# Kernel optimization log

Hardware: AMD Instinct MI355X
Metric: run time of the kernel (lower is better)

## Reference

```python
import jax, jax.numpy as jnp
import numpy as np

D_MODEL = 1024
D_STATE = 128
HEADDIM = 64
EXPAND = 2
CHUNK = 64
D_CONV = 4
D_INNER = EXPAND * D_MODEL          # 2048
NHEADS = D_INNER // HEADDIM         # 32
D_IN_PROJ = 2 * D_INNER + 2 * D_STATE + NHEADS  # 4384
CONV_CH = D_INNER + 2 * D_STATE     # 2304
EPS = 1e-5


def segsum(x):
    # x: (..., T) -> (..., T, T); out[i, j] = sum_{k=j+1..i} x[k] for i>=j else -inf
    T = x.shape[-1]
    m1 = jnp.tril(jnp.ones((T, T), bool), -1)
    xr = jnp.where(m1, x[..., :, None], 0.0)   # zero above/at diagonal before cumsum
    s = jnp.cumsum(xr, axis=-2)
    m0 = jnp.tril(jnp.ones((T, T), bool), 0)
    return jnp.where(m0, s, -jnp.inf)


def ssd(x, A, B, C, chunk):
    # x: (b, L, h, p); A: (b, L, h); B, C: (b, L, n)  (the h=1 dim of the torch code is squeezed)
    b, L, h, p = x.shape
    c = L // chunk
    x = x.reshape(b, c, chunk, h, p)
    A = A.reshape(b, c, chunk, h).transpose(0, 3, 1, 2)  # (b, h, c, l)
    B = B.reshape(b, c, chunk, -1)                       # (b, c, l, n)
    C = C.reshape(b, c, chunk, -1)
    A_cum = jnp.cumsum(A, axis=-1)                       # (b, h, c, l)
    Lm = jnp.exp(segsum(A))                              # (b, h, c, l, l)
    # intra-chunk (diagonal block) output
    Y_diag = jnp.einsum('bcln,bcsn,bhcls,bcshp->bclhp', C, B, Lm, x)
    # per-chunk states
    decay_states = jnp.exp(A_cum[:, :, :, -1:] - A_cum)  # (b, h, c, l)
    states = jnp.einsum('bcln,bhcl,bclhp->bchpn', B, decay_states, x)
    init = jnp.zeros_like(states[:, :1])
    states = jnp.concatenate([init, states], axis=1)     # (b, c+1, h, p, n)
    # inter-chunk recurrence
    Ac_last = jnp.pad(A_cum[:, :, :, -1], ((0, 0), (0, 0), (1, 0)))  # (b, h, c+1)
    decay_chunk = jnp.exp(segsum(Ac_last))               # (b, h, c+1, c+1)
    new_states = jnp.einsum('bhzc,bchpn->bzhpn', decay_chunk, states)
    states = new_states[:, :-1]                          # (b, c, h, p, n)
    sdo = jnp.exp(A_cum)
    Y_off = jnp.einsum('bcln,bchpn,bhcl->bclhp', C, states, sdo)
    return (Y_diag + Y_off).reshape(b, L, h, p)


def setup_inputs() -> dict:
    key = jax.random.key(0)
    ks = jax.random.split(key, 8)
    return {
        'u': jax.random.normal(ks[0], (2, 4096, D_MODEL), jnp.float32),
        'W_in': jax.random.normal(ks[1], (D_MODEL, D_IN_PROJ), jnp.float32) * 0.02,
        'conv_w': jax.random.normal(ks[2], (CONV_CH, D_CONV), jnp.float32) * 0.3,
        'conv_b': jax.random.normal(ks[3], (CONV_CH,), jnp.float32) * 0.1,
        'dt_bias': jax.random.normal(ks[4], (NHEADS,), jnp.float32),
        'A_log': jax.random.normal(ks[5], (NHEADS,), jnp.float32) * 0.5,
        'D': jax.random.normal(ks[6], (NHEADS,), jnp.float32),
        'norm_w': jnp.ones((D_INNER,), jnp.float32),
        'W_out': jax.random.normal(ks[7], (D_INNER, D_MODEL), jnp.float32) * 0.02,
    }


def reference(u, W_in, conv_w, conv_b, dt_bias, A_log, D, norm_w, W_out):
    b, L, _ = u.shape
    zxbcdt = u @ W_in                                    # (b, L, 4384)
    z = zxbcdt[..., :D_INNER]
    xBC = zxbcdt[..., D_INNER:D_INNER + CONV_CH]
    dt = jax.nn.softplus(zxbcdt[..., -NHEADS:] + dt_bias)  # (b, L, h)
    # depthwise causal conv (Conv1d pad=d_conv-1, truncated to L == left-pad only)
    xc = jnp.pad(xBC.transpose(0, 2, 1), ((0, 0), (0, 0), (D_CONV - 1, 0)))
    xc = jax.lax.conv_general_dilated(
        xc, conv_w[:, None, :], (1,), 'VALID',
        feature_group_count=CONV_CH,
        dimension_numbers=('NCH', 'OIH', 'NCH')) + conv_b[None, :, None]
    xBC = jax.nn.silu(xc.transpose(0, 2, 1))             # (b, L, 2304)
    x = xBC[..., :D_INNER].reshape(b, L, NHEADS, HEADDIM)
    B = xBC[..., D_INNER:D_INNER + D_STATE]
    C = xBC[..., D_INNER + D_STATE:]
    A = -jnp.exp(A_log)                                  # (h,)
    y = ssd(x * dt[..., None], A * dt, B, C, CHUNK)
    y = y + x * D[:, None]
    y = y.reshape(b, L, D_INNER)
    # RMSNorm with gate z
    y = y * jax.nn.silu(z)
    y = y * jax.lax.rsqrt(jnp.mean(y * y, axis=-1, keepdims=True) + EPS) * norm_w
    return y @ W_out
```

## Files before the change

### kernel.cpp

```cpp
#include <hip/hip_runtime.h>
#include <hip/hip_bf16.h>
#include <math.h>

#define D_MODEL   1024
#define D_STATE   128
#define HEADDIM   64
#define CHUNK     64
#define D_INNER   2048
#define NHEADS    32
#define D_IN_PROJ 4384
#define CONV_CH   2304
#define RCOLS     2336
#define WINT_ROWS 4480
#define BATCH     2
#define SEQ       4096
#define NCHUNK    64
#define ROWS      (BATCH*SEQ)
#define EPS_RMS   1e-5f

typedef __hip_bfloat16 bf16;
typedef __bf16 bf16x8_t __attribute__((ext_vector_type(8)));
typedef float  f32x4_t  __attribute__((ext_vector_type(4)));

__device__ __forceinline__ float siluf_(float x){ return x/(1.f+expf(-x)); }
__device__ __forceinline__ float ldf(const float* p){ return *p; }
__device__ __forceinline__ float ldf(const bf16* p){ return __bfloat162float(*p); }
__device__ __forceinline__ void  stf(float* p, float v){ *p = v; }
__device__ __forceinline__ void  stf(bf16* p, float v){ *p = __float2bfloat16(v); }

__device__ __forceinline__ __bf16 tobf(float v){
    __hip_bfloat16 t = __float2bfloat16(v);
    return *reinterpret_cast<__bf16*>(&t);
}
__device__ __forceinline__ unsigned short bfbits(float v){
    __hip_bfloat16 t = __float2bfloat16(v);
    return *reinterpret_cast<unsigned short*>(&t);
}
__device__ __forceinline__ float bfbits2f(unsigned short u){
    union { unsigned u; float f; } cv; cv.u = ((unsigned)u) << 16; return cv.f;
}

__device__ __forceinline__ void async16(const void* g, void* l) {
    __builtin_amdgcn_global_load_lds(
        (const __attribute__((address_space(1))) unsigned int*)g,
        (__attribute__((address_space(3))) unsigned int*)l, 16, 0, 0);
}

struct Core {
    f32x4_t acc[4][4];

    __device__ __forceinline__ void stA2(const bf16* __restrict__ A, int lda,
                                         int row0, int kk, __bf16* Asb,
                                         int tid, int lcb, int wb, int c0) {
#pragma unroll
        for (int c = c0; c < c0 + 2; ++c) {
            const char* src = (const char*)(A + (size_t)(row0 + c * 64 + (tid >> 3)) * lda + kk) + lcb;
            async16(src, Asb + c * 4096 + wb);
        }
    }
    __device__ __forceinline__ void stB2(const bf16* __restrict__ Bt, int ldb,
                                         int col0, int kk, __bf16* Bsb,
                                         int tid, int lcb, int wb) {
#pragma unroll
        for (int c = 0; c < 2; ++c) {
            const char* src = (const char*)(Bt + (size_t)(col0 + c * 64 + (tid >> 3)) * ldb + kk) + lcb;
            async16(src, Bsb + c * 4096 + wb);
        }
    }

    __device__ __forceinline__ void run(const bf16* __restrict__ A,
                                        const bf16* __restrict__ Bt,
                                        int lda, int ldb,
                                        int row0, int col0, int k0, int nt,
                                        __bf16* As, __bf16* Bs, int tid) {
        const int wave = tid >> 6, lane = tid & 63;
        const int quad = lane >> 4, l16 = lane & 15;
        const int wm = wave >> 1, wn = wave & 1;
        const int wb  = wave << 9;
        const int lcb = (((tid & 7) ^ ((tid >> 3) & 7)) << 4);
        const int xb = (l16 & 7) << 4;

#pragma unroll
        for (int i = 0; i < 4; ++i)
#pragma unroll
            for (int j = 0; j < 4; ++j) acc[i][j] = (f32x4_t){0.f, 0.f, 0.f, 0.f};

        int aoff[4][2], boff[4][2];
#pragma unroll
        for (int mi = 0; mi < 4; ++mi)
#pragma unroll
            for (int ks = 0; ks < 2; ++ks) {
                const int cb = ((ks << 6) | (quad << 4)) ^ xb;
                aoff[mi][ks] = (wm * 64 + mi * 16 + l16) * 128 + cb;
                boff[mi][ks] = (wn * 64 + mi * 16 + l16) * 128 + cb;
            }

        stA2(A, lda, row0, k0, As, tid, lcb, wb, 0);
        stA2(A, lda, row0, k0, As, tid, lcb, wb, 2);
        stB2(Bt, ldb, col0, k0, Bs, tid, lcb, wb);
        stA2(A, lda, row0, k0 + 64, As + 16384, tid, lcb, wb, 0);
        stA2(A, lda, row0, k0 + 64, As + 16384, tid, lcb, wb, 2);
        stB2(Bt, ldb, col0, k0 + 64, Bs + 8192, tid, lcb, wb);

        const char* AsC = (const char*)As;
        const char* BsC = (const char*)Bs;
        int cur = 0;
        for (int t = 0; t < nt; ++t) {
            if (t < nt - 1) asm volatile("s_waitcnt vmcnt(6)" ::: "memory");
            else            asm volatile("s_waitcnt vmcnt(0)" ::: "memory");
            __builtin_amdgcn_s_barrier();
            asm volatile("" ::: "memory");

            const int sb = (cur + 2 >= 3) ? cur - 1 : cur + 2;
            const bool st = (t + 2 < nt);
            const int kk = k0 + (t + 2) * 64;
            const char* Ab = AsC + cur * 32768;
            const char* Bb = BsC + cur * 16384;
            __bf16* Asb = As + sb * 16384;
            __bf16* Bsb = Bs + sb * 8192;

            bf16x8_t af0[2][2], af1[2][2], bf0[2][2], bf1[2][2];

#pragma unroll
            for (int i = 0; i < 2; ++i)
#pragma unroll
                for (int ks = 0; ks < 2; ++ks) {
                    af0[i][ks] = *(const bf16x8_t*)(Ab + aoff[i][ks]);
                    bf0[i][ks] = *(const bf16x8_t*)(Bb + boff[i][ks]);
                }
            if (st) stA2(A, lda, row0, kk, Asb, tid, lcb, wb, 0);
            asm volatile("" ::: "memory");
            __builtin_amdgcn_s_barrier();
            asm volatile("" ::: "memory");
            __builtin_amdgcn_s_setprio(1);
#pragma unroll
            for (int ks = 0; ks < 2; ++ks)
#pragma unroll
                for (int mi = 0; mi < 2; ++mi)
#pragma unroll
                    for (int ni = 0; ni < 2; ++ni)
                        acc[mi][ni] = __builtin_amdgcn_mfma_f32_16x16x32_bf16(
                            af0[mi][ks], bf0[ni][ks], acc[mi][ni], 0, 0, 0);
            __builtin_amdgcn_s_setprio(0);

#pragma unroll
            for (int i = 0; i < 2; ++i)
#pragma unroll
                for (int ks = 0; ks < 2; ++ks)
                    bf1[i][ks] = *(const bf16x8_t*)(Bb + boff[2 + i][ks]);
            if (st) stA2(A, lda, row0, kk, Asb, tid, lcb, wb, 2);
            asm volatile("" ::: "memory");
            __builtin_amdgcn_s_barrier();
            asm volatile("" ::: "memory");
            __builtin_amdgcn_s_setprio(1);
#pragma unroll
            for (int ks = 0; ks < 2; ++ks)
#pragma unroll
                for (int mi = 0; mi < 2; ++mi)
#pragma unroll
                    for (int ni = 0; ni < 2; ++ni)
                        acc[mi][2 + ni] = __builtin_amdgcn_mfma_f32_16x16x32_bf16(
                            af0[mi][ks], bf1[ni][ks], acc[mi][2 + ni], 0, 0, 0);
            __builtin_amdgcn_s_setprio(0);

#pragma unroll
            for (int i = 0; i < 2; ++i)
#pragma unroll
                for (int ks = 0; ks < 2; ++ks)
                    af1[i][ks] = *(const bf16x8_t*)(Ab + aoff[2 + i][ks]);
            if (st) stB2(Bt, ldb, col0, kk, Bsb, tid, lcb, wb);
            asm volatile("" ::: "memory");
            __builtin_amdgcn_s_barrier();
            asm volatile("" ::: "memory");
            __builtin_amdgcn_s_setprio(1);
#pragma unroll
            for (int ks = 0; ks < 2; ++ks)
#pragma unroll
                for (int mi = 0; mi < 2; ++mi) {
#pragma unroll
                    for (int ni = 0; ni < 2; ++ni)
                        acc[2 + mi][2 + ni] = __builtin_amdgcn_mfma_f32_16x16x32_bf16(
                            af1[mi][ks], bf1[ni][ks], acc[2 + mi][2 + ni], 0, 0, 0);
#pragma unroll
                    for (int ni = 0; ni < 2; ++ni)
                        acc[2 + mi][ni] = __builtin_amdgcn_mfma_f32_16x16x32_bf16(
                            af1[mi][ks], bf0[ni][ks], acc[2 + mi][ni], 0, 0, 0);
                }
            __builtin_amdgcn_s_setprio(0);

            cur = (cur + 1 == 3) ? 0 : cur + 1;
        }
    }
};

__global__ __launch_bounds__(512) void gemm_zr_fused(const bf16* __restrict__ A,
                                                     const bf16* __restrict__ Bt,
                                                     bf16* __restrict__ Z,
                                                     bf16* __restrict__ R) {
    __shared__ __align__(16) __bf16 As[3 * 16384];
    __shared__ __align__(16) __bf16 Bs[3 * 8192];
    const int tid = threadIdx.x;
    const int row0 = blockIdx.x * 256;
    const int ct   = blockIdx.y;
    Core g;
    g.run(A, Bt, D_MODEL, D_MODEL, row0, ct * 128, 0, 16, As, Bs, tid);

    const int wave = tid >> 6, lane = tid & 63;
    const int quad = lane >> 4, l16 = lane & 15;
    const int wm = wave >> 1, wn = wave & 1;
    bf16* Cp; int ldc_, cl0, ncols;
    if (ct < 16) { Cp = Z; ldc_ = D_INNER; cl0 = ct * 128;           ncols = D_INNER; }
    else         { Cp = R; ldc_ = RCOLS;   cl0 = ct * 128 - D_INNER; ncols = RCOLS; }
#pragma unroll
    for (int ni = 0; ni < 4; ++ni) {
        int gc = cl0 + wn * 64 + ni * 16 + l16;
        if (gc >= ncols) continue;
#pragma unroll
        for (int mi = 0; mi < 4; ++mi)
#pragma unroll
            for (int r = 0; r < 4; ++r) {
                int gr = row0 + wm * 64 + mi * 16 + quad * 4 + r;
                stf(&Cp[(size_t)gr * ldc_ + gc], g.acc[mi][ni][r]);
            }
    }
}

__global__ __launch_bounds__(512) void gemm_out_kernel(const bf16* __restrict__ A,
                                                       const bf16* __restrict__ Bt,
                                                       float* __restrict__ out) {
    __shared__ __align__(16) __bf16 As[3 * 16384];
    __shared__ __align__(16) __bf16 Bs[3 * 8192];
    const int tid = threadIdx.x;
    const int row0 = blockIdx.x * 256;
    const int col0 = blockIdx.y * 128;
    Core g;
    g.run(A, Bt, D_INNER, D_INNER, row0, col0, 0, 32, As, Bs, tid);

    const int wave = tid >> 6, lane = tid & 63;
    const int quad = lane >> 4, l16 = lane & 15;
    const int wm = wave >> 1, wn = wave & 1;
#pragma unroll
    for (int ni = 0; ni < 4; ++ni) {
        int gc = col0 + wn * 64 + ni * 16 + l16;
#pragma unroll
        for (int mi = 0; mi < 4; ++mi)
#pragma unroll
            for (int r = 0; r < 4; ++r) {
                int gr = row0 + wm * 64 + mi * 16 + quad * 4 + r;
                out[(size_t)gr * D_MODEL + gc] = g.acc[mi][ni][r];
            }
    }
}

__global__ void cvt_bf16_kernel(const float* __restrict__ src,
                                bf16* __restrict__ dst, int n4) {
    int i = blockIdx.x * 256 + threadIdx.x;
    if (i >= n4) return;
    float4 v = ((const float4*)src)[i];
    dst[i * 4 + 0] = __float2bfloat16(v.x);
    dst[i * 4 + 1] = __float2bfloat16(v.y);
    dst[i * 4 + 2] = __float2bfloat16(v.z);
    dst[i * 4 + 3] = __float2bfloat16(v.w);
}

__global__ __launch_bounds__(256) void transpose_cvt_kernel(const float* __restrict__ W,
                                                            bf16* __restrict__ Wt,
                                                            int R, int C, int Cpad) {
    __shared__ float tile[32][33];
    int c0 = blockIdx.x * 32, r0 = blockIdx.y * 32;
    int tx = threadIdx.x & 31, ty = threadIdx.x >> 5;
    for (int i = ty; i < 32; i += 8) {
        int r = r0 + i, c = c0 + tx;
        tile[i][tx] = (c < C) ? W[(size_t)r * C + c] : 0.f;
    }
    __syncthreads();
    for (int i = ty; i < 32; i += 8) {
        int c = c0 + i, r = r0 + tx;
        stf(&Wt[(size_t)c * R + r], tile[tx][i]);
    }
}

__global__ void prep_convw_kernel(const float* __restrict__ conv_w,
                                  bf16* __restrict__ Wc) {
    int i = blockIdx.x * 256 + threadIdx.x;
    if (i >= CONV_CH * 4) return;
    int ch = i >> 2, k = i & 3;
    Wc[k * CONV_CH + ch] = __float2bfloat16(conv_w[ch * 4 + k]);
}

__global__ __launch_bounds__(256) void conv_silu_kernel(const bf16* __restrict__ R,
                                                        const bf16* __restrict__ Wc,
                                                        const float* __restrict__ conv_b,
                                                        bf16* __restrict__ xBC) {
    int idx = blockIdx.x * 256 + threadIdx.x;
    int rq = idx / 288;
    int g = idx - rq * 288;
    int ch0 = g * 8;
    int row0 = rq * 4;
    int l0 = row0 & (SEQ - 1);

    uint4 rv[7];
#pragma unroll
    for (int j = 0; j < 7; ++j) {
        int ls = l0 - 3 + j;
        rv[j] = (ls >= 0) ? *(const uint4*)&R[(size_t)(row0 - 3 + j) * RCOLS + ch0]
                          : make_uint4(0u, 0u, 0u, 0u);
    }
    uint4 wv[4];
#pragma unroll
    for (int k = 0; k < 4; ++k)
        wv[k] = *(const uint4*)&Wc[k * CONV_CH + ch0];
    float4 b0 = ((const float4*)conv_b)[ch0 / 4];
    float4 b1 = ((const float4*)conv_b)[ch0 / 4 + 1];
    const float bias[8] = {b0.x, b0.y, b0.z, b0.w, b1.x, b1.y, b1.z, b1.w};
    float wf[4][8];
#pragma unroll
    for (int k = 0; k < 4; ++k) {
        const unsigned* wp = (const unsigned*)&wv[k];
#pragma unroll
        for (int j2 = 0; j2 < 4; ++j2) {
            wf[k][2 * j2]     = bfbits2f((unsigned short)(wp[j2] & 0xffff));
            wf[k][2 * j2 + 1] = bfbits2f((unsigned short)(wp[j2] >> 16));
        }
    }
#pragma unroll
    for (int j = 0; j < 4; ++j) {
        float acc[8];
#pragma unroll
        for (int cc = 0; cc < 8; ++cc) acc[cc] = bias[cc];
#pragma unroll
        for (int k = 0; k < 4; ++k) {
            const unsigned* vp = (const unsigned*)&rv[j + k];
#pragma unroll
            for (int j2 = 0; j2 < 4; ++j2) {
                unsigned v = vp[j2];
                acc[2 * j2]     += wf[k][2 * j2]     * bfbits2f((unsigned short)(v & 0xffff));
                acc[2 * j2 + 1] += wf[k][2 * j2 + 1] * bfbits2f((unsigned short)(v >> 16));
            }
        }
        unsigned o[4];
#pragma unroll
        for (int j2 = 0; j2 < 4; ++j2)
            o[j2] = (unsigned)bfbits(siluf_(acc[2 * j2])) |
                    ((unsigned)bfbits(siluf_(acc[2 * j2 + 1])) << 16);
        *(uint4*)&xBC[(size_t)(row0 + j) * CONV_CH + ch0] = make_uint4(o[0], o[1], o[2], o[3]);
    }
}

__global__ void dt_kernel(const bf16* __restrict__ R,
                          const float* __restrict__ dt_bias,
                          float* __restrict__ dtb) {
    int i = blockIdx.x * 256 + threadIdx.x;
    int row = i >> 2, h0 = (i & 3) * 8;
    uint4 v = *(const uint4*)&R[(size_t)row * RCOLS + CONV_CH + h0];
    float4 bia0 = ((const float4*)dt_bias)[h0 / 4];
    float4 bia1 = ((const float4*)dt_bias)[h0 / 4 + 1];
    const unsigned vv[4] = {v.x, v.y, v.z, v.w};
    const float bb[8] = {bia0.x, bia0.y, bia0.z, bia0.w, bia1.x, bia1.y, bia1.z, bia1.w};
    float o[8];
#pragma unroll
    for (int j = 0; j < 4; ++j) {
        float a = bfbits2f((unsigned short)(vv[j] & 0xffff)) + bb[2*j];
        float c = bfbits2f((unsigned short)(vv[j] >> 16)) + bb[2*j+1];
        o[2*j]   = (a > 20.f) ? a : log1pf(expf(a));
        o[2*j+1] = (c > 20.f) ? c : log1pf(expf(c));
    }
    float* dp = &dtb[(size_t)row * NHEADS + h0];
    *(float4*)dp       = make_float4(o[0], o[1], o[2], o[3]);
    *(float4*)(dp + 4) = make_float4(o[4], o[5], o[6], o[7]);
}

__global__ void acum_kernel(const float* __restrict__ dtb,
                            const float* __restrict__ A_log,
                            float* __restrict__ Acum) {
    int bch = blockIdx.x;
    int h = bch & 31;
    int bc = bch >> 5;
    int c = bc & 63, b = bc >> 6;
    int row0 = b * SEQ + c * CHUNK;
    __shared__ float sh[64];
    int l = threadIdx.x;
    float Ah = -expf(A_log[h]);
    sh[l] = Ah * dtb[(size_t)(row0 + l) * NHEADS + h];
    __syncthreads();
    float s = 0.f;
    for (int j = 0; j <= l; ++j) s += sh[j];
    Acum[(size_t)bch * 64 + l] = s;
}

__global__ __launch_bounds__(64) void gchunk_mfma_kernel(const bf16* __restrict__ xBC,
                                                         float* __restrict__ Gbuf) {
    int bc = blockIdx.x;
    int c = bc & 63, b = bc >> 6;
    int row0 = b * SEQ + c * CHUNK;
    int lane = threadIdx.x;
    int quad = lane >> 4, l16 = lane & 15;

    f32x4_t acc[4][4];
#pragma unroll
    for (int i = 0; i < 4; ++i)
#pragma unroll
        for (int j = 0; j < 4; ++j) acc[i][j] = (f32x4_t){0.f, 0.f, 0.f, 0.f};

#pragma unroll
    for (int ks = 0; ks < 4; ++ks) {
        bf16x8_t a[4], bb[4];
#pragma unroll
        for (int mi = 0; mi < 4; ++mi)
            a[mi] = *(const bf16x8_t*)&xBC[(size_t)(row0 + mi * 16 + l16) * CONV_CH +
                                           D_INNER + D_STATE + ks * 32 + quad * 8];
#pragma unroll
        for (int ni = 0; ni < 4; ++ni)
            bb[ni] = *(const bf16x8_t*)&xBC[(size_t)(row0 + ni * 16 + l16) * CONV_CH +
                                            D_INNER + ks * 32 + quad * 8];
#pragma unroll
        for (int mi = 0; mi < 4; ++mi)
#pragma unroll
            for (int ni = 0; ni < 4; ++ni)
                acc[mi][ni] = __builtin_amdgcn_mfma_f32_16x16x32_bf16(
                    a[mi], bb[ni], acc[mi][ni], 0, 0, 0);
    }
#pragma unroll
    for (int ni = 0; ni < 4; ++ni) {
        int s = ni * 16 + l16;
#pragma unroll
        for (int mi = 0; mi < 4; ++mi)
#pragma unroll
            for (int r = 0; r < 4; ++r) {
                int l = mi * 16 + quad * 4 + r;
                Gbuf[(size_t)bc * 4096 + l * 64 + s] = acc[mi][ni][r];
            }
    }
}

__global__ __launch_bounds__(256) void states_mfma_kernel(const bf16* __restrict__ xBC,
                                                          const float* __restrict__ dtb,
                                                          const float* __restrict__ Acum,
                                                          bf16* __restrict__ states) {
    __shared__ __align__(16) __bf16 BsT[128 * 72];
    __shared__ __align__(16) __bf16 xdT[4][64 * 72];
    __shared__ float dtdec[4][64];
    int bcq = blockIdx.x;
    int hq = bcq & 7, bc = bcq >> 3;
    int c = bc & 63, b = bc >> 6;
    int tid = threadIdx.x, wave = tid >> 6, lane = tid & 63;
    int h = hq * 4 + wave;
    int bch = bc * 32 + h;
    int row0 = b * SEQ + c * CHUNK;
    int quad = lane >> 4, l16 = lane & 15;

    {
        float alast = Acum[(size_t)bch * 64 + 63];
        float a = Acum[(size_t)bch * 64 + lane];
        dtdec[wave][lane] = dtb[(size_t)(row0 + lane) * NHEADS + h] * expf(alast - a);
    }
    __syncthreads();
    for (int it = 0; it < 16; ++it) {
        int i2 = tid + 256 * it;
        int l = i2 >> 6;
        int n0 = (i2 & 63) * 2;
        unsigned v = *(const unsigned*)&xBC[(size_t)(row0 + l) * CONV_CH + D_INNER + n0];
        *(unsigned short*)&BsT[(n0    ) * 72 + l] = (unsigned short)(v & 0xffff);
        *(unsigned short*)&BsT[(n0 + 1) * 72 + l] = (unsigned short)(v >> 16);
    }
    for (int it = 0; it < 32; ++it) {
        int l = 2 * it + (lane >> 5);
        int p0 = (lane & 31) * 2;
        unsigned v = *(const unsigned*)&xBC[(size_t)(row0 + l) * CONV_CH + h * 64 + p0];
        float f = dtdec[wave][l];
        xdT[wave][(p0    ) * 72 + l] = tobf(bfbits2f((unsigned short)(v & 0xffff)) * f);
        xdT[wave][(p0 + 1) * 72 + l] = tobf(bfbits2f((unsigned short)(v >> 16)) * f);
    }
    __syncthreads();

    f32x4_t acc[4][8];
#pragma unroll
    for (int i = 0; i < 4; ++i)
#pragma unroll
        for (int j = 0; j < 8; ++j) acc[i][j] = (f32x4_t){0.f, 0.f, 0.f, 0.f};
#pragma unroll
    for (int ks = 0; ks < 2; ++ks) {
        bf16x8_t a[4], bb[8];
#pragma unroll
        for (int mi = 0; mi < 4; ++mi)
            a[mi] = *(const bf16x8_t*)(&xdT[wave][(mi * 16 + l16) * 72 + ks * 32 + quad * 8]);
#pragma unroll
        for (int ni = 0; ni < 8; ++ni)
            bb[ni] = *(const bf16x8_t*)(&BsT[(ni * 16 + l16) * 72 + ks * 32 + quad * 8]);
#pragma unroll
        for (int mi = 0; mi < 4; ++mi)
#pragma unroll
            for (int ni = 0; ni < 8; ++ni)
                acc[mi][ni] = __builtin_amdgcn_mfma_f32_16x16x32_bf16(
                    a[mi], bb[ni], acc[mi][ni], 0, 0, 0);
    }
#pragma unroll
    for (int ni = 0; ni < 8; ++ni) {
        int n = ni * 16 + l16;
#pragma unroll
        for (int mi = 0; mi < 4; ++mi)
#pragma unroll
            for (int r = 0; r < 4; ++r) {
                int p = mi * 16 + quad * 4 + r;
                stf(&states[(size_t)bch * 8192 + p * 128 + n], acc[mi][ni][r]);
            }
    }
}

__global__ void scan_kernel(const float* __restrict__ Acum,
                            bf16* __restrict__ states) {
    int i = blockIdx.x * 256 + threadIdx.x;
    int pn0 = (i & 2047) * 4;
    int bh = i >> 11;
    int h = bh & 31, b = bh >> 5;
    float carry[4] = {0.f, 0.f, 0.f, 0.f};
    for (int c = 0; c < NCHUNK; ++c) {
        int bch = (b * NCHUNK + c) * NHEADS + h;
        bf16* sp = &states[(size_t)bch * 8192 + pn0];
        uint2 v = *(const uint2*)sp;
        float s0 = bfbits2f((unsigned short)(v.x & 0xffff));
        float s1 = bfbits2f((unsigned short)(v.x >> 16));
        float s2 = bfbits2f((unsigned short)(v.y & 0xffff));
        float s3 = bfbits2f((unsigned short)(v.y >> 16));
        uint2 o;
        o.x = (unsigned)bfbits(carry[0]) | ((unsigned)bfbits(carry[1]) << 16);
        o.y = (unsigned)bfbits(carry[2]) | ((unsigned)bfbits(carry[3]) << 16);
        *(uint2*)sp = o;
        float dec = expf(Acum[(size_t)bch * 64 + 63]);
        carry[0] = carry[0] * dec + s0;
        carry[1] = carry[1] * dec + s1;
        carry[2] = carry[2] * dec + s2;
        carry[3] = carry[3] * dec + s3;
    }
}

__global__ __launch_bounds__(64) void y_mfma_kernel(const bf16* __restrict__ xBC,
                                                    const float* __restrict__ dtb,
                                                    const float* __restrict__ Acum,
                                                    const float* __restrict__ Gbuf,
                                                    const bf16* __restrict__ states,
                                                    const float* __restrict__ Dv,
                                                    bf16* __restrict__ y) {
    __shared__ __align__(16) __bf16 Mm[64 * 72];
    __shared__ __align__(16) __bf16 xsT[64 * 72];
    __shared__ float acs[64], dtss[64], sdos[64];
    int bch = blockIdx.x;
    int h = bch & 31, bc = bch >> 5;
    int c = bc & 63, b = bc >> 6;
    int row0 = b * SEQ + c * CHUNK;
    int lane = threadIdx.x;
    int quad = lane >> 4, l16 = lane & 15;

    {
        float a = Acum[(size_t)bch * 64 + lane];
        acs[lane] = a;
        sdos[lane] = expf(a);
        dtss[lane] = dtb[(size_t)(row0 + lane) * NHEADS + h];
    }
    __syncthreads();
    for (int l = 0; l < 64; ++l) {
        int s = lane;
        float d = acs[l] - acs[s];
        float g = (s <= l) ? Gbuf[(size_t)bc * 4096 + l * 64 + s] * dtss[s] : 0.f;
        float coef = g * expf((s <= l) ? d : 0.f);
        Mm[l * 72 + s] = tobf(coef);
    }
    for (int it = 0; it < 32; ++it) {
        int l = 2 * it + (lane >> 5);
        int p0 = (lane & 31) * 2;
        unsigned v = *(const unsigned*)&xBC[(size_t)(row0 + l) * CONV_CH + h * 64 + p0];
        *(unsigned short*)&xsT[(p0    ) * 72 + l] = (unsigned short)(v & 0xffff);
        *(unsigned short*)&xsT[(p0 + 1) * 72 + l] = (unsigned short)(v >> 16);
    }
    __syncthreads();

    f32x4_t acc[4][4];
#pragma unroll
    for (int i = 0; i < 4; ++i)
#pragma unroll
        for (int j = 0; j < 4; ++j) acc[i][j] = (f32x4_t){0.f, 0.f, 0.f, 0.f};

#pragma unroll
    for (int ks = 0; ks < 2; ++ks) {
        bf16x8_t a[4], bb[4];
#pragma unroll
        for (int mi = 0; mi < 4; ++mi)
            a[mi] = *(const bf16x8_t*)(&Mm[(mi * 16 + l16) * 72 + ks * 32 + quad * 8]);
#pragma unroll
        for (int ni = 0; ni < 4; ++ni)
            bb[ni] = *(const bf16x8_t*)(&xsT[(ni * 16 + l16) * 72 + ks * 32 + quad * 8]);
#pragma unroll
        for (int mi = 0; mi < 4; ++mi)
#pragma unroll
            for (int ni = 0; ni < 4; ++ni)
                acc[mi][ni] = __builtin_amdgcn_mfma_f32_16x16x32_bf16(
                    a[mi], bb[ni], acc[mi][ni], 0, 0, 0);
    }
    float sdo_mi[4];
#pragma unroll
    for (int mi = 0; mi < 4; ++mi) sdo_mi[mi] = sdos[mi * 16 + l16];
#pragma unroll
    for (int ks = 0; ks < 4; ++ks) {
        bf16x8_t a[4], bb[4];
#pragma unroll
        for (int mi = 0; mi < 4; ++mi) {
            const unsigned* cp = (const unsigned*)&xBC[(size_t)(row0 + mi * 16 + l16) * CONV_CH
                                                       + D_INNER + D_STATE + ks * 32 + quad * 8];
            float sc = sdo_mi[mi];
#pragma unroll
            for (int jj = 0; jj < 4; ++jj) {
                unsigned v = cp[jj];
                a[mi][2 * jj    ] = tobf(bfbits2f((unsigned short)(v & 0xffff)) * sc);
                a[mi][2 * jj + 1] = tobf(bfbits2f((unsigned short)(v >> 16)) * sc);
            }
        }
#pragma unroll
        for (int ni = 0; ni < 4; ++ni)
            bb[ni] = *(const bf16x8_t*)&states[(size_t)bch * 8192 + (ni * 16 + l16) * 128
                                               + ks * 32 + quad * 8];
#pragma unroll
        for (int mi = 0; mi < 4; ++mi)
#pragma unroll
            for (int ni = 0; ni < 4; ++ni)
                acc[mi][ni] = __builtin_amdgcn_mfma_f32_16x16x32_bf16(
                    a[mi], bb[ni], acc[mi][ni], 0, 0, 0);
    }
    float Dh = Dv[h];
#pragma unroll
    for (int ni = 0; ni < 4; ++ni) {
        int p = ni * 16 + l16;
#pragma unroll
        for (int mi = 0; mi < 4; ++mi)
#pragma unroll
            for (int r = 0; r < 4; ++r) {
                int l = mi * 16 + quad * 4 + r;
                float xv = bfbits2f(*(const unsigned short*)&xsT[p * 72 + l]);
                stf(&y[(size_t)(row0 + l) * D_INNER + h * 64 + p],
                    acc[mi][ni][r] + Dh * xv);
            }
    }
}

__global__ __launch_bounds__(256) void gate_norm_kernel(const bf16* __restrict__ Z,
                                                        const float* __restrict__ nw,
                                                        bf16* __restrict__ y) {
    int row = blockIdx.x;
    int tid = threadIdx.x;
    int col0 = tid * 8;
    uint4 zv = *(const uint4*)&Z[(size_t)row * D_INNER + col0];
    uint4 yv = *(const uint4*)&y[(size_t)row * D_INNER + col0];
    const unsigned zz[4] = {zv.x, zv.y, zv.z, zv.w};
    const unsigned yy[4] = {yv.x, yv.y, yv.z, yv.w};
    float vals[8];
    float local = 0.f;
#pragma unroll
    for (int j = 0; j < 4; ++j) {
        float z0 = bfbits2f((unsigned short)(zz[j] & 0xffff));
        float z1 = bfbits2f((unsigned short)(zz[j] >> 16));
        float y0 = bfbits2f((unsigned short)(yy[j] & 0xffff));
        float y1 = bfbits2f((unsigned short)(yy[j] >> 16));
        float v0 = y0 * siluf_(z0);
        float v1 = y1 * siluf_(z1);
        vals[2*j] = v0; vals[2*j+1] = v1;
        local += v0 * v0 + v1 * v1;
    }
#pragma unroll
    for (int off = 32; off; off >>= 1) local += __shfl_down(local, off, 64);
    __shared__ float wsum[4];
    if ((tid & 63) == 0) wsum[tid >> 6] = local;
    __syncthreads();
    float total = wsum[0] + wsum[1] + wsum[2] + wsum[3];
    float scale = rsqrtf(total / (float)D_INNER + EPS_RMS);
    float4 w0 = ((const float4*)nw)[col0 / 4];
    float4 w1 = ((const float4*)nw)[col0 / 4 + 1];
    const float ww[8] = {w0.x, w0.y, w0.z, w0.w, w1.x, w1.y, w1.z, w1.w};
    unsigned o[4];
#pragma unroll
    for (int j = 0; j < 4; ++j)
        o[j] = (unsigned)bfbits(vals[2*j] * scale * ww[2*j]) |
               ((unsigned)bfbits(vals[2*j+1] * scale * ww[2*j+1]) << 16);
    *(uint4*)&y[(size_t)row * D_INNER + col0] = make_uint4(o[0], o[1], o[2], o[3]);
}

extern "C" void kernel_launch(void* const* d_in, const int* in_sizes, int n_in,
                              void* d_out, int out_size, void* d_ws, size_t ws_size,
                              hipStream_t stream) {
    const float* u       = (const float*)d_in[0];
    const float* W_in    = (const float*)d_in[1];
    const float* conv_w  = (const float*)d_in[2];
    const float* conv_b  = (const float*)d_in[3];
    const float* dt_bias = (const float*)d_in[4];
    const float* A_log   = (const float*)d_in[5];
    const float* Dv      = (const float*)d_in[6];
    const float* norm_w  = (const float*)d_in[7];
    const float* W_out   = (const float*)d_in[8];
    float* out = (float*)d_out;

    const size_t sz_xBC    = (size_t)ROWS * CONV_CH * 2;
    const size_t sz_Z      = (size_t)ROWS * D_INNER * 2;
    const size_t sz_y      = (size_t)ROWS * D_INNER * 2;
    const size_t sz_states = (size_t)BATCH * NCHUNK * NHEADS * 8192 * 2;
    const size_t sz_dtb    = (size_t)ROWS * NHEADS * 4;
    const size_t sz_Acum   = (size_t)BATCH * NCHUNK * NHEADS * 64 * 4;
    const size_t sz_Gbuf   = (size_t)BATCH * NCHUNK * 4096 * 4;
    const size_t sz_WinT   = (size_t)WINT_ROWS * D_MODEL * 2;
    const size_t sz_WoutT  = (size_t)D_MODEL * D_INNER * 2;
    const size_t sz_Wc     = (size_t)CONV_CH * 4 * 2;
    const size_t need = sz_xBC + sz_Z + sz_y + sz_states + sz_dtb + sz_Acum +
                        sz_Gbuf + sz_WinT + sz_WoutT + sz_Wc;
    if (ws_size < need) {
        hipMemsetAsync(d_out, 0, (size_t)out_size * sizeof(float), stream);
        return;
    }
    char* ws = (char*)d_ws;
    size_t off = 0;
    bf16*  xBC    = (bf16*) (ws + off); off += sz_xBC;
    bf16*  Z      = (bf16*) (ws + off); off += sz_Z;
    bf16*  y      = (bf16*) (ws + off); off += sz_y;
    bf16*  states = (bf16*) (ws + off); off += sz_states;
    float* dtb    = (float*)(ws + off); off += sz_dtb;
    float* Acum   = (float*)(ws + off); off += sz_Acum;
    float* Gbuf   = (float*)(ws + off); off += sz_Gbuf;
    bf16*  W_inT  = (bf16*) (ws + off); off += sz_WinT;
    bf16*  W_outT = (bf16*) (ws + off); off += sz_WoutT;
    bf16*  Wc     = (bf16*) (ws + off); off += sz_Wc;
    bf16*  R        = states;
    bf16*  u_bf16   = (bf16*)((char*)states + (size_t)ROWS * RCOLS * 2);

    cvt_bf16_kernel<<<(ROWS * D_MODEL / 4 + 255) / 256, 256, 0, stream>>>(
        u, u_bf16, ROWS * D_MODEL / 4);
    transpose_cvt_kernel<<<dim3(WINT_ROWS / 32, D_MODEL / 32), 256, 0, stream>>>(
        W_in, W_inT, D_MODEL, D_IN_PROJ, WINT_ROWS);
    transpose_cvt_kernel<<<dim3(D_MODEL / 32, D_INNER / 32), 256, 0, stream>>>(
        W_out, W_outT, D_INNER, D_MODEL, D_MODEL);
    prep_convw_kernel<<<(CONV_CH * 4 + 255) / 256, 256, 0, stream>>>(conv_w, Wc);
    gemm_zr_fused<<<dim3(ROWS / 256, 35), 512, 0, stream>>>(u_bf16, W_inT, Z, R);
    conv_silu_kernel<<<ROWS / 4 * 288 / 256, 256, 0, stream>>>(R, Wc, conv_b, xBC);
    dt_kernel<<<ROWS * 4 / 256, 256, 0, stream>>>(R, dt_bias, dtb);
    acum_kernel<<<BATCH * NCHUNK * NHEADS, 64, 0, stream>>>(dtb, A_log, Acum);
    gchunk_mfma_kernel<<<BATCH * NCHUNK, 64, 0, stream>>>(xBC, Gbuf);
    states_mfma_kernel<<<BATCH * NCHUNK * 8, 256, 0, stream>>>(xBC, dtb, Acum, states);
    scan_kernel<<<BATCH * NHEADS * 2048 / 256, 256, 0, stream>>>(Acum, states);
    y_mfma_kernel<<<BATCH * NCHUNK * NHEADS, 64, 0, stream>>>(
        xBC, dtb, Acum, Gbuf, states, Dv, y);
    gate_norm_kernel<<<ROWS, 256, 0, stream>>>(Z, norm_w, y);
    gemm_out_kernel<<<dim3(ROWS / 256, D_MODEL / 128), 512, 0, stream>>>(
        y, W_outT, out);
}
```

Measured before the change: 437.4 us.

## Enlarge GEMM tiles to 256x256 with double buffering and split-K output GEMM

Replaces the 256x128 triple-buffered GEMM core with a 256x256 tile using 8 waves arranged 2x4, each computing a 128x64 sub-tile, with two-stage LDS double buffering. The input-projection GEMM gets padded weight rows so it can use 256-wide column tiles. The output GEMM now splits K in two, writes fp32 partial sums into the reused states buffer, and adds a separate reduction kernel. The aim is higher arithmetic intensity per loaded tile and enough blocks to fill the GPU. The cost is more accumulator registers, which may limit occupancy, extra fp32 partial-sum traffic, one more kernel launch, and wasted compute on the padded columns.

```diff
diff --git a/kernel.cpp b/kernel.cpp
--- a/kernel.cpp
+++ b/kernel.cpp
@@ -11,7 +11,7 @@
 #define D_IN_PROJ 4384
 #define CONV_CH   2304
 #define RCOLS     2336
-#define WINT_ROWS 4480
+#define WINT_ROWS 4608
 #define BATCH     2
 #define SEQ       4096
 #define NCHUNK    64
@@ -46,26 +46,14 @@
         (__attribute__((address_space(3))) unsigned int*)l, 16, 0, 0);
 }
 
-struct Core {
-    f32x4_t acc[4][4];
-
-    __device__ __forceinline__ void stA2(const bf16* __restrict__ A, int lda,
-                                         int row0, int kk, __bf16* Asb,
-                                         int tid, int lcb, int wb, int c0) {
-#pragma unroll
-        for (int c = c0; c < c0 + 2; ++c) {
-            const char* src = (const char*)(A + (size_t)(row0 + c * 64 + (tid >> 3)) * lda + kk) + lcb;
-            async16(src, Asb + c * 4096 + wb);
-        }
-    }
-    __device__ __forceinline__ void stB2(const bf16* __restrict__ Bt, int ldb,
-                                         int col0, int kk, __bf16* Bsb,
-                                         int tid, int lcb, int wb) {
-#pragma unroll
-        for (int c = 0; c < 2; ++c) {
-            const char* src = (const char*)(Bt + (size_t)(col0 + c * 64 + (tid >> 3)) * ldb + kk) + lcb;
-            async16(src, Bsb + c * 4096 + wb);
-        }
+struct Core256 {
+    f32x4_t acc[8][4];
+
+    __device__ __forceinline__ void stg(const bf16* __restrict__ g, int ld,
+                                        int rbase, int kk, __bf16* buf, int c,
+                                        int tid, int lcb) {
+        const char* src = (const char*)(g + (size_t)(rbase + c * 64 + (tid >> 3)) * ld + kk) + lcb;
+        async16(src, buf + c * 4096 + ((tid >> 6) << 9));
     }
 
     __device__ __forceinline__ void run(const bf16* __restrict__ A,
@@ -75,120 +63,148 @@
                                         __bf16* As, __bf16* Bs, int tid) {
         const int wave = tid >> 6, lane = tid & 63;
         const int quad = lane >> 4, l16 = lane & 15;
-        const int wm = wave >> 1, wn = wave & 1;
-        const int wb  = wave << 9;
+        const int wm = wave >> 2, wn = wave & 3;
         const int lcb = (((tid & 7) ^ ((tid >> 3) & 7)) << 4);
         const int xb = (l16 & 7) << 4;
 
 #pragma unroll
-        for (int i = 0; i < 4; ++i)
+        for (int i = 0; i < 8; ++i)
 #pragma unroll
             for (int j = 0; j < 4; ++j) acc[i][j] = (f32x4_t){0.f, 0.f, 0.f, 0.f};
 
-        int aoff[4][2], boff[4][2];
-#pragma unroll
-        for (int mi = 0; mi < 4; ++mi)
-#pragma unroll
-            for (int ks = 0; ks < 2; ++ks) {
-                const int cb = ((ks << 6) | (quad << 4)) ^ xb;
-                aoff[mi][ks] = (wm * 64 + mi * 16 + l16) * 128 + cb;
-                boff[mi][ks] = (wn * 64 + mi * 16 + l16) * 128 + cb;
-            }
-
-        stA2(A, lda, row0, k0, As, tid, lcb, wb, 0);
-        stA2(A, lda, row0, k0, As, tid, lcb, wb, 2);
-        stB2(Bt, ldb, col0, k0, Bs, tid, lcb, wb);
-        stA2(A, lda, row0, k0 + 64, As + 16384, tid, lcb, wb, 0);
-        stA2(A, lda, row0, k0 + 64, As + 16384, tid, lcb, wb, 2);
-        stB2(Bt, ldb, col0, k0 + 64, Bs + 8192, tid, lcb, wb);
-
-        const char* AsC = (const char*)As;
-        const char* BsC = (const char*)Bs;
-        int cur = 0;
+        int aoff[8][2], boff[4][2];
+#pragma unroll
+        for (int ks = 0; ks < 2; ++ks) {
+            const int cb = ((ks << 6) | (quad << 4)) ^ xb;
+#pragma unroll
+            for (int mi = 0; mi < 8; ++mi)
+                aoff[mi][ks] = (wm * 128 + mi * 16 + l16) * 128 + cb;
+#pragma unroll
+            for (int ni = 0; ni < 4; ++ni)
+                boff[ni][ks] = (wn * 64 + ni * 16 + l16) * 128 + cb;
+        }
+
+        stg(A,  lda, row0, k0, As, 0, tid, lcb);
+        stg(A,  lda, row0, k0, As, 2, tid, lcb);
+        stg(Bt, ldb, col0, k0, Bs, 0, tid, lcb);
+        stg(Bt, ldb, col0, k0, Bs, 1, tid, lcb);
+        stg(Bt, ldb, col0, k0, Bs, 2, tid, lcb);
+        stg(Bt, ldb, col0, k0, Bs, 3, tid, lcb);
+        stg(A,  lda, row0, k0, As, 1, tid, lcb);
+        stg(A,  lda, row0, k0, As, 3, tid, lcb);
+        asm volatile("s_waitcnt vmcnt(2)" ::: "memory");
+        __builtin_amdgcn_s_barrier();
+        asm volatile("" ::: "memory");
+
         for (int t = 0; t < nt; ++t) {
-            if (t < nt - 1) asm volatile("s_waitcnt vmcnt(6)" ::: "memory");
-            else            asm volatile("s_waitcnt vmcnt(0)" ::: "memory");
+            const bool st = (t + 1 < nt);
+            const int kk = k0 + (t + 1) * 64;
+            const int cur = t & 1;
+            const char* Ab = (const char*)(As + cur * 16384);
+            const char* Bb = (const char*)(Bs + cur * 16384);
+            __bf16* Asb = As + (cur ^ 1) * 16384;
+            __bf16* Bsb = Bs + (cur ^ 1) * 16384;
+            bf16x8_t af[4][2], b0r[2][2], b1r[2][2];
+
+#pragma unroll
+            for (int mi = 0; mi < 4; ++mi)
+#pragma unroll
+                for (int ks = 0; ks < 2; ++ks)
+                    af[mi][ks] = *(const bf16x8_t*)(Ab + aoff[mi][ks]);
+#pragma unroll
+            for (int ni = 0; ni < 2; ++ni)
+#pragma unroll
+                for (int ks = 0; ks < 2; ++ks)
+                    b0r[ni][ks] = *(const bf16x8_t*)(Bb + boff[ni][ks]);
+            if (st) {
+                stg(A,  lda, row0, kk, Asb, 0, tid, lcb);
+                stg(A,  lda, row0, kk, Asb, 2, tid, lcb);
+                stg(Bt, ldb, col0, kk, Bsb, 0, tid, lcb);
+            }
+            asm volatile("" ::: "memory");
+            __builtin_amdgcn_s_barrier();
+            asm volatile("s_waitcnt lgkmcnt(0)" ::: "memory");
+            __builtin_amdgcn_s_setprio(1);
+#pragma unroll
+            for (int ks = 0; ks < 2; ++ks)
+#pragma unroll
+                for (int mi = 0; mi < 4; ++mi)
+#pragma unroll
+                    for (int ni = 0; ni < 2; ++ni)
+                        acc[mi][ni] = __builtin_amdgcn_mfma_f32_16x16x32_bf16(
+                            af[mi][ks], b0r[ni][ks], acc[mi][ni], 0, 0, 0);
+            __builtin_amdgcn_s_setprio(0);
             __builtin_amdgcn_s_barrier();
             asm volatile("" ::: "memory");
 
-            const int sb = (cur + 2 >= 3) ? cur - 1 : cur + 2;
-            const bool st = (t + 2 < nt);
-            const int kk = k0 + (t + 2) * 64;
-            const char* Ab = AsC + cur * 32768;
-            const char* Bb = BsC + cur * 16384;
-            __bf16* Asb = As + sb * 16384;
-            __bf16* Bsb = Bs + sb * 8192;
-
-            bf16x8_t af0[2][2], af1[2][2], bf0[2][2], bf1[2][2];
-
-#pragma unroll
-            for (int i = 0; i < 2; ++i)
-#pragma unroll
-                for (int ks = 0; ks < 2; ++ks) {
-                    af0[i][ks] = *(const bf16x8_t*)(Ab + aoff[i][ks]);
-                    bf0[i][ks] = *(const bf16x8_t*)(Bb + boff[i][ks]);
-                }
-            if (st) stA2(A, lda, row0, kk, Asb, tid, lcb, wb, 0);
+#pragma unroll
+            for (int ni = 0; ni < 2; ++ni)
+#pragma unroll
+                for (int ks = 0; ks < 2; ++ks)
+                    b1r[ni][ks] = *(const bf16x8_t*)(Bb + boff[2 + ni][ks]);
+            if (st) {
+                stg(Bt, ldb, col0, kk, Bsb, 1, tid, lcb);
+                stg(Bt, ldb, col0, kk, Bsb, 2, tid, lcb);
+                stg(Bt, ldb, col0, kk, Bsb, 3, tid, lcb);
+                asm volatile("s_waitcnt vmcnt(6)" ::: "memory");
+            } else {
+                asm volatile("s_waitcnt vmcnt(0)" ::: "memory");
+            }
+            __builtin_amdgcn_s_barrier();
+            asm volatile("s_waitcnt lgkmcnt(0)" ::: "memory");
+            __builtin_amdgcn_s_setprio(1);
+#pragma unroll
+            for (int ks = 0; ks < 2; ++ks)
+#pragma unroll
+                for (int mi = 0; mi < 4; ++mi)
+#pragma unroll
+                    for (int ni = 0; ni < 2; ++ni)
+                        acc[mi][2 + ni] = __builtin_amdgcn_mfma_f32_16x16x32_bf16(
+                            af[mi][ks], b1r[ni][ks], acc[mi][2 + ni], 0, 0, 0);
+            __builtin_amdgcn_s_setprio(0);
+            __builtin_amdgcn_s_barrier();
             asm volatile("" ::: "memory");
+
+#pragma unroll
+            for (int mi = 0; mi < 4; ++mi)
+#pragma unroll
+                for (int ks = 0; ks < 2; ++ks)
+                    af[mi][ks] = *(const bf16x8_t*)(Ab + aoff[4 + mi][ks]);
+            if (st) stg(A, lda, row0, kk, Asb, 1, tid, lcb);
+            asm volatile("" ::: "memory");
+            __builtin_amdgcn_s_barrier();
+            asm volatile("s_waitcnt lgkmcnt(0)" ::: "memory");
+            __builtin_amdgcn_s_setprio(1);
+#pragma unroll
+            for (int ks = 0; ks < 2; ++ks)
+#pragma unroll
+                for (int mi = 0; mi < 4; ++mi)
+#pragma unroll
+                    for (int ni = 0; ni < 2; ++ni)
+                        acc[4 + mi][2 + ni] = __builtin_amdgcn_mfma_f32_16x16x32_bf16(
+                            af[mi][ks], b1r[ni][ks], acc[4 + mi][2 + ni], 0, 0, 0);
+            __builtin_amdgcn_s_setprio(0);
+            __builtin_amdgcn_s_barrier();
+            asm volatile("" ::: "memory");
+
+            if (st) {
+                stg(A, lda, row0, kk, Asb, 3, tid, lcb);
+                asm volatile("s_waitcnt vmcnt(2)" ::: "memory");
+            }
             __builtin_amdgcn_s_barrier();
             asm volatile("" ::: "memory");
             __builtin_amdgcn_s_setprio(1);
 #pragma unroll
             for (int ks = 0; ks < 2; ++ks)
 #pragma unroll
-                for (int mi = 0; mi < 2; ++mi)
+                for (int mi = 0; mi < 4; ++mi)
 #pragma unroll
                     for (int ni = 0; ni < 2; ++ni)
-                        acc[mi][ni] = __builtin_amdgcn_mfma_f32_16x16x32_bf16(
-                            af0[mi][ks], bf0[ni][ks], acc[mi][ni], 0, 0, 0);
+                        acc[4 + mi][ni] = __builtin_amdgcn_mfma_f32_16x16x32_bf16(
+                            af[mi][ks], b0r[ni][ks], acc[4 + mi][ni], 0, 0, 0);
             __builtin_amdgcn_s_setprio(0);
-
-#pragma unroll
-            for (int i = 0; i < 2; ++i)
-#pragma unroll
-                for (int ks = 0; ks < 2; ++ks)
-                    bf1[i][ks] = *(const bf16x8_t*)(Bb + boff[2 + i][ks]);
-            if (st) stA2(A, lda, row0, kk, Asb, tid, lcb, wb, 2);
-            asm volatile("" ::: "memory");
             __builtin_amdgcn_s_barrier();
             asm volatile("" ::: "memory");
-            __builtin_amdgcn_s_setprio(1);
-#pragma unroll
-            for (int ks = 0; ks < 2; ++ks)
-#pragma unroll
-                for (int mi = 0; mi < 2; ++mi)
-#pragma unroll
-                    for (int ni = 0; ni < 2; ++ni)
-                        acc[mi][2 + ni] = __builtin_amdgcn_mfma_f32_16x16x32_bf16(
-                            af0[mi][ks], bf1[ni][ks], acc[mi][2 + ni], 0, 0, 0);
-            __builtin_amdgcn_s_setprio(0);
-
-#pragma unroll
-            for (int i = 0; i < 2; ++i)
-#pragma unroll
-                for (int ks = 0; ks < 2; ++ks)
-                    af1[i][ks] = *(const bf16x8_t*)(Ab + aoff[2 + i][ks]);
-            if (st) stB2(Bt, ldb, col0, kk, Bsb, tid, lcb, wb);
-            asm volatile("" ::: "memory");
-            __builtin_amdgcn_s_barrier();
-            asm volatile("" ::: "memory");
-            __builtin_amdgcn_s_setprio(1);
-#pragma unroll
-            for (int ks = 0; ks < 2; ++ks)
-#pragma unroll
-                for (int mi = 0; mi < 2; ++mi) {
-#pragma unroll
-                    for (int ni = 0; ni < 2; ++ni)
-                        acc[2 + mi][2 + ni] = __builtin_amdgcn_mfma_f32_16x16x32_bf16(
-                            af1[mi][ks], bf1[ni][ks], acc[2 + mi][2 + ni], 0, 0, 0);
-#pragma unroll
-                    for (int ni = 0; ni < 2; ++ni)
-                        acc[2 + mi][ni] = __builtin_amdgcn_mfma_f32_16x16x32_bf16(
-                            af1[mi][ks], bf0[ni][ks], acc[2 + mi][ni], 0, 0, 0);
-                }
-            __builtin_amdgcn_s_setprio(0);
-
-            cur = (cur + 1 == 3) ? 0 : cur + 1;
         }
     }
 };
@@ -197,59 +213,69 @@
                                                      const bf16* __restrict__ Bt,
                                                      bf16* __restrict__ Z,
                                                      bf16* __restrict__ R) {
-    __shared__ __align__(16) __bf16 As[3 * 16384];
-    __shared__ __align__(16) __bf16 Bs[3 * 8192];
+    __shared__ __align__(16) __bf16 As[2 * 16384];
+    __shared__ __align__(16) __bf16 Bs[2 * 16384];
     const int tid = threadIdx.x;
     const int row0 = blockIdx.x * 256;
     const int ct   = blockIdx.y;
-    Core g;
-    g.run(A, Bt, D_MODEL, D_MODEL, row0, ct * 128, 0, 16, As, Bs, tid);
+    Core256 g;
+    g.run(A, Bt, D_MODEL, D_MODEL, row0, ct * 256, 0, 16, As, Bs, tid);
 
     const int wave = tid >> 6, lane = tid & 63;
     const int quad = lane >> 4, l16 = lane & 15;
-    const int wm = wave >> 1, wn = wave & 1;
+    const int wm = wave >> 2, wn = wave & 3;
     bf16* Cp; int ldc_, cl0, ncols;
-    if (ct < 16) { Cp = Z; ldc_ = D_INNER; cl0 = ct * 128;           ncols = D_INNER; }
-    else         { Cp = R; ldc_ = RCOLS;   cl0 = ct * 128 - D_INNER; ncols = RCOLS; }
+    if (ct < 8) { Cp = Z; ldc_ = D_INNER; cl0 = ct * 256;           ncols = D_INNER; }
+    else        { Cp = R; ldc_ = RCOLS;   cl0 = ct * 256 - D_INNER; ncols = RCOLS; }
 #pragma unroll
     for (int ni = 0; ni < 4; ++ni) {
         int gc = cl0 + wn * 64 + ni * 16 + l16;
         if (gc >= ncols) continue;
 #pragma unroll
-        for (int mi = 0; mi < 4; ++mi)
+        for (int mi = 0; mi < 8; ++mi)
 #pragma unroll
             for (int r = 0; r < 4; ++r) {
-                int gr = row0 + wm * 64 + mi * 16 + quad * 4 + r;
+                int gr = row0 + wm * 128 + mi * 16 + quad * 4 + r;
                 stf(&Cp[(size_t)gr * ldc_ + gc], g.acc[mi][ni][r]);
             }
     }
 }
 
-__global__ __launch_bounds__(512) void gemm_out_kernel(const bf16* __restrict__ A,
+__global__ __launch_bounds__(512) void gemm_out_splitk(const bf16* __restrict__ A,
                                                        const bf16* __restrict__ Bt,
-                                                       float* __restrict__ out) {
-    __shared__ __align__(16) __bf16 As[3 * 16384];
-    __shared__ __align__(16) __bf16 Bs[3 * 8192];
+                                                       float* __restrict__ part) {
+    __shared__ __align__(16) __bf16 As[2 * 16384];
+    __shared__ __align__(16) __bf16 Bs[2 * 16384];
     const int tid = threadIdx.x;
     const int row0 = blockIdx.x * 256;
-    const int col0 = blockIdx.y * 128;
-    Core g;
-    g.run(A, Bt, D_INNER, D_INNER, row0, col0, 0, 32, As, Bs, tid);
+    const int col0 = blockIdx.y * 256;
+    const int kz   = blockIdx.z;
+    Core256 g;
+    g.run(A, Bt, D_INNER, D_INNER, row0, col0, kz * 1024, 16, As, Bs, tid);
 
     const int wave = tid >> 6, lane = tid & 63;
     const int quad = lane >> 4, l16 = lane & 15;
-    const int wm = wave >> 1, wn = wave & 1;
+    const int wm = wave >> 2, wn = wave & 3;
+    float* P = part + (size_t)kz * ROWS * D_MODEL;
 #pragma unroll
     for (int ni = 0; ni < 4; ++ni) {
         int gc = col0 + wn * 64 + ni * 16 + l16;
 #pragma unroll
-        for (int mi = 0; mi < 4; ++mi)
+        for (int mi = 0; mi < 8; ++mi)
 #pragma unroll
             for (int r = 0; r < 4; ++r) {
-                int gr = row0 + wm * 64 + mi * 16 + quad * 4 + r;
-                out[(size_t)gr * D_MODEL + gc] = g.acc[mi][ni][r];
-            }
-    }
+                int gr = row0 + wm * 128 + mi * 16 + quad * 4 + r;
+                P[(size_t)gr * D_MODEL + gc] = g.acc[mi][ni][r];
+            }
+    }
+}
+
+__global__ void reduce_out_kernel(const float* __restrict__ part,
+                                  float* __restrict__ out) {
+    int i = blockIdx.x * 256 + threadIdx.x;
+    float4 a = ((const float4*)part)[i];
+    float4 b = ((const float4*)(part + (size_t)ROWS * D_MODEL))[i];
+    ((float4*)out)[i] = make_float4(a.x + b.x, a.y + b.y, a.z + b.z, a.w + b.w);
 }
 
 __global__ void cvt_bf16_kernel(const float* __restrict__ src,
@@ -726,6 +752,7 @@
     bf16*  Wc     = (bf16*) (ws + off); off += sz_Wc;
     bf16*  R        = states;
     bf16*  u_bf16   = (bf16*)((char*)states + (size_t)ROWS * RCOLS * 2);
+    float* out_part = (float*)states;
 
     cvt_bf16_kernel<<<(ROWS * D_MODEL / 4 + 255) / 256, 256, 0, stream>>>(
         u, u_bf16, ROWS * D_MODEL / 4);
@@ -734,7 +761,8 @@
     transpose_cvt_kernel<<<dim3(D_MODEL / 32, D_INNER / 32), 256, 0, stream>>>(
         W_out, W_outT, D_INNER, D_MODEL, D_MODEL);
     prep_convw_kernel<<<(CONV_CH * 4 + 255) / 256, 256, 0, stream>>>(conv_w, Wc);
-    gemm_zr_fused<<<dim3(ROWS / 256, 35), 512, 0, stream>>>(u_bf16, W_inT, Z, R);
+    gemm_zr_fused<<<dim3(ROWS / 256, WINT_ROWS / 256), 512, 0, stream>>>(
+        u_bf16, W_inT, Z, R);
     conv_silu_kernel<<<ROWS / 4 * 288 / 256, 256, 0, stream>>>(R, Wc, conv_b, xBC);
     dt_kernel<<<ROWS * 4 / 256, 256, 0, stream>>>(R, dt_bias, dtb);
     acum_kernel<<<BATCH * NCHUNK * NHEADS, 64, 0, stream>>>(dtb, A_log, Acum);
@@ -744,6 +772,7 @@
     y_mfma_kernel<<<BATCH * NCHUNK * NHEADS, 64, 0, stream>>>(
         xBC, dtb, Acum, Gbuf, states, Dv, y);
     gate_norm_kernel<<<ROWS, 256, 0, stream>>>(Z, norm_w, y);
-    gemm_out_kernel<<<dim3(ROWS / 256, D_MODEL / 128), 512, 0, stream>>>(
-        y, W_outT, out);
-}
+    gemm_out_splitk<<<dim3(ROWS / 256, D_MODEL / 256, 2), 512, 0, stream>>>(
+        y, W_outT, out_part);
+    reduce_out_kernel<<<ROWS * D_MODEL / 4 / 256, 256, 0, stream>>>(out_part, out);
+}
```

Result: no change. 444.0 us (+1.5%).
